# Optimization experiments

Measured on AMD Instinct MI355X. Metric: run time of the kernel, lower is better.

## Reference

```python
import jax, jax.numpy as jnp
import numpy as np
import math

B, T, N, E = 16, 12, 2000, 8000
D, GAT_HEADS, NHEAD, FF, L, HORIZON = 64, 4, 4, 128, 2, 3
M = B * N  # batched node count


def setup_inputs() -> dict:
    key = jax.random.key(0)
    ks = jax.random.split(key, 16)

    def nrm(k, shape, s=0.1):
        return jax.random.normal(k, shape, jnp.float32) * s

    return dict(
        x_seq=jax.random.normal(ks[0], (B, T, N), jnp.float32),
        edge_index=jax.random.randint(ks[1], (2, E), 0, N),
        # GATConv 1: in_dim=1 -> 4 heads x 8 = 32
        W1=nrm(ks[2], (1, 32)),
        att_src1=nrm(ks[3], (GAT_HEADS, 8)),
        att_dst1=nrm(ks[4], (GAT_HEADS, 8)),
        b1=jnp.zeros((32,), jnp.float32),
        # GATConv 2: 32 -> 4 heads x 16 = 64
        W2=nrm(ks[5], (32, 64)),
        att_src2=nrm(ks[6], (GAT_HEADS, 16)),
        att_dst2=nrm(ks[7], (GAT_HEADS, 16)),
        b2=jnp.zeros((64,), jnp.float32),
        # TransformerEncoder (post-LN, relu), stacked over L layers
        Wqkv=nrm(ks[8], (L, 3 * D, D)), bqkv=jnp.zeros((L, 3 * D), jnp.float32),
        Wo=nrm(ks[9], (L, D, D)), bo=jnp.zeros((L, D), jnp.float32),
        Wf1=nrm(ks[10], (L, FF, D)), bf1=jnp.zeros((L, FF), jnp.float32),
        Wf2=nrm(ks[11], (L, D, FF)), bf2=jnp.zeros((L, D), jnp.float32),
        g1=jnp.ones((L, D), jnp.float32), be1=jnp.zeros((L, D), jnp.float32),
        g2=jnp.ones((L, D), jnp.float32), be2=jnp.zeros((L, D), jnp.float32),
        # prediction head
        Wh=nrm(ks[12], (HORIZON, D)), bh=jnp.zeros((HORIZON,), jnp.float32),
    )


def _layer_norm(x, g, b, eps=1e-5):
    mu = x.mean(-1, keepdims=True)
    var = ((x - mu) ** 2).mean(-1, keepdims=True)
    return (x - mu) * jax.lax.rsqrt(var + eps) * g + b


def _gat(x, src, dst, W, a_src, a_dst, bias, H, C, num_nodes):
    # PyG GATConv (concat=True, eval mode). x: [M, in] -> [M, H*C]
    h = (x @ W).reshape(-1, H, C)                                  # [M,H,C]
    e = jax.nn.leaky_relu((h * a_src).sum(-1)[src] + (h * a_dst).sum(-1)[dst], 0.2)  # [Etot,H]
    m = jax.ops.segment_max(e, dst, num_segments=num_nodes)
    w = jnp.exp(e - m[dst])
    s = jax.ops.segment_sum(w, dst, num_segments=num_nodes)
    alpha = w / (s[dst] + 1e-16)
    out = jax.ops.segment_sum(h[src] * alpha[:, :, None], dst, num_segments=num_nodes)
    return out.reshape(-1, H * C) + bias


def _forward(x_seq, edge_index, W1, att_src1, att_dst1, b1, W2, att_src2, att_dst2, b2,
             Wqkv, bqkv, Wo, bo, Wf1, bf1, Wf2, bf2, g1, be1, g2, be2, Wh, bh):
    # batch edge index with per-graph node offsets, then add self loops (PyG default)
    offs = (jnp.arange(B) * N)[:, None]
    loops = jnp.arange(M)
    src = jnp.concatenate([(edge_index[0][None] + offs).reshape(-1), loops])
    dst = jnp.concatenate([(edge_index[1][None] + offs).reshape(-1), loops])

    xt = x_seq.transpose(1, 0, 2).reshape(T, M, 1)  # per-timestep node features

    def gnn_step(x):
        h = jax.nn.relu(_gat(x, src, dst, W1, att_src1, att_dst1, b1, GAT_HEADS, 8, M))
        return jax.nn.relu(_gat(h, src, dst, W2, att_src2, att_dst2, b2, GAT_HEADS, 16, M))

    seq = jax.vmap(gnn_step)(xt)  # [T, M, D]

    # sinusoidal positional encoding over time axis
    pos = jnp.arange(T, dtype=jnp.float32)[:, None]
    div = jnp.exp(jnp.arange(0, D, 2, dtype=jnp.float32) * (-math.log(10000.0) / D))
    pe = jnp.zeros((T, D), jnp.float32)
    pe = pe.at[:, 0::2].set(jnp.sin(pos * div)).at[:, 1::2].set(jnp.cos(pos * div))
    seq = seq + pe[:, None, :]

    hd = D // NHEAD
    scale = 1.0 / math.sqrt(hd)
    for i in range(L):  # post-LN transformer encoder layers
        qkv = seq @ Wqkv[i].T + bqkv[i]
        q, k, v = jnp.split(qkv, 3, axis=-1)
        q = q.reshape(T, M, NHEAD, hd)
        k = k.reshape(T, M, NHEAD, hd)
        v = v.reshape(T, M, NHEAD, hd)
        sc = jnp.einsum('tmhd,smhd->mhts', q, k) * scale  # [M,H,T,T]
        attn = jax.nn.softmax(sc, axis=-1)
        o = jnp.einsum('mhts,smhd->tmhd', attn, v).reshape(T, M, D)
        seq = _layer_norm(seq + (o @ Wo[i].T + bo[i]), g1[i], be1[i])
        ff = jax.nn.relu(seq @ Wf1[i].T + bf1[i]) @ Wf2[i].T + bf2[i]
        seq = _layer_norm(seq + ff, g2[i], be2[i])

    final = seq[-1]  # [M, D]
    return (final @ Wh.T + bh).reshape(B, N, HORIZON).transpose(0, 2, 1)  # [B, horizon, N]


def reference(x_seq, edge_index, W1, att_src1, att_dst1, b1, W2, att_src2, att_dst2, b2,
              Wqkv, bqkv, Wo, bo, Wf1, bf1, Wf2, bf2, g1, be1, g2, be2, Wh, bh):
    return _forward(x_seq, edge_index, W1, att_src1, att_dst1, b1, W2, att_src2, att_dst2, b2,
                    Wqkv, bqkv, Wo, bo, Wf1, bf1, Wf2, bf2, g1, be1, g2, be2, Wh, bh)
```

## Files before the change

### kernel.cpp

```cpp
#include <hip/hip_runtime.h>
#include <hip/hip_bf16.h>

#define B_ 16
#define T_ 12
#define N_ 2000
#define E_ 8000
#define M_ 32000
#define ETOT (B_*E_ + M_)
#define D_ 64

typedef __hip_bfloat16 bf16;
typedef unsigned short u16;
typedef __attribute__((ext_vector_type(8))) _Float16 half8;
typedef __attribute__((ext_vector_type(2))) _Float16 h2v;
typedef __attribute__((ext_vector_type(4))) float f32x4;

__device__ __forceinline__ float bfu(u16 u){ return __uint_as_float(((unsigned int)u)<<16); }
__device__ __forceinline__ u16 f2bu(float f){
  unsigned int x = __float_as_uint(f);
  x += 0x7FFFu + ((x >> 16) & 1u);
  return (u16)(x >> 16);
}
__device__ __forceinline__ u16 f2h(float f){
  _Float16 h = (_Float16)f; u16 r; __builtin_memcpy(&r, &h, 2); return r;
}
__device__ __forceinline__ float h2f(u16 u){
  _Float16 h; __builtin_memcpy(&h, &u, 2); return (float)h;
}
__device__ __forceinline__ h2v u2h(unsigned u){ h2v r; __builtin_memcpy(&r,&u,4); return r; }

__global__ void k_prep(const float* __restrict__ Wqkv, const float* __restrict__ Wo,
                       const float* __restrict__ Wf1, const float* __restrict__ Wf2,
                       u16* __restrict__ wqB, u16* __restrict__ woB,
                       u16* __restrict__ w1B, u16* __restrict__ w2B,
                       float* __restrict__ peT){
  int i = blockIdx.x*256 + threadIdx.x;
  if(i < 24576){
    int l=i/12288, r=i-l*12288;
    int nt=r>>10, r2=r&1023, c=r2>>9, r3=r2&511, lane=r3>>3, jj=r3&7;
    int m=lane&15, q=lane>>4;
    wqB[i] = f2h(Wqkv[l*12288 + (nt*16+m)*64 + c*32 + q*8 + jj]);
  } else if(i < 32768){
    int k2=i-24576;
    int l=k2>>12, r=k2&4095;
    int nt=r>>10, r2=r&1023, c=r2>>9, r3=r2&511, lane=r3>>3, jj=r3&7;
    int m=lane&15, q=lane>>4;
    woB[k2] = f2h(Wo[l*4096 + (nt*16+m)*64 + c*32 + q*8 + jj]);
  } else if(i < 49152){
    int k2=i-32768;
    int l=k2>>13, r=k2&8191;
    int nt=r>>10, r2=r&1023, c=r2>>9, r3=r2&511, lane=r3>>3, jj=r3&7;
    int m=lane&15, q=lane>>4;
    w1B[k2] = f2h(Wf1[l*8192 + (nt*16+m)*64 + c*32 + q*8 + jj]);
  } else if(i < 65536){
    int k2=i-49152;
    int l=k2>>13, r=k2&8191;
    int nt=r>>11, r2=r&2047, c=r2>>9, r3=r2&511, lane=r3>>3, jj=r3&7;
    int m=lane&15, q=lane>>4;
    w2B[k2] = f2h(Wf2[l*8192 + (nt*16+m)*128 + c*32 + q*8 + jj]);
  } else {
    int i2 = i - 65536;
    if(i2 < 768){
      int t=i2>>6, ch=i2&63;
      float ang = (float)t * __expf(-0.14391156463f * (float)(ch & ~1));
      peT[i2] = (ch&1) ? __cosf(ang) : __sinf(ang);
    }
  }
}

__global__ void k_hist(const int* __restrict__ ei, int* __restrict__ deg){
  int e = blockIdx.x*256 + threadIdx.x; if(e>=ETOT) return;
  int dst;
  if (e < B_*E_){ int b = e / E_; int k = e - b*E_; dst = ei[E_ + k] + b*N_; }
  else dst = e - B_*E_;
  atomicAdd(&deg[dst], 1);
}

__global__ void k_scan1(const int* __restrict__ deg, int* __restrict__ offs, int* __restrict__ bsums){
  __shared__ int s[256];
  int tid = threadIdx.x; int g = blockIdx.x*256 + tid;
  s[tid] = deg[g]; __syncthreads();
  for(int off=1; off<256; off<<=1){
    int a = (tid>=off) ? s[tid-off] : 0; __syncthreads();
    s[tid] += a; __syncthreads();
  }
  offs[g+1] = s[tid];
  if(tid==255) bsums[blockIdx.x] = s[255];
}

__global__ void k_scan2(const int* __restrict__ bsums, int* __restrict__ boffs){
  __shared__ int s[128];
  int tid = threadIdx.x;
  int v = (tid<125) ? bsums[tid] : 0;
  s[tid] = v; __syncthreads();
  for(int off=1; off<128; off<<=1){
    int a = (tid>=off) ? s[tid-off] : 0; __syncthreads();
    s[tid] += a; __syncthreads();
  }
  if(tid<125) boffs[tid] = s[tid] - v;
}

__global__ void k_scan3(int* __restrict__ offs, const int* __restrict__ boffs){
  int tid = threadIdx.x; int g = blockIdx.x*256 + tid;
  offs[g+1] += boffs[blockIdx.x];
  if(g==0) offs[0]=0;
}

__global__ void k_scatter(const int* __restrict__ ei, const int* __restrict__ offs,
                          int* __restrict__ cursor, int* __restrict__ csr){
  int e = blockIdx.x*256 + threadIdx.x; if(e>=ETOT) return;
  int srcl, dst;
  if (e < B_*E_){ int b=e/E_; int k=e-b*E_; srcl=ei[k]; dst=ei[E_+k]+b*N_; }
  else { dst = e - B_*E_; int b=dst/N_; srcl = dst - b*N_; }
  int pos = atomicAdd(&cursor[dst], 1);
  csr[offs[dst]+pos] = srcl;
}

__global__ __launch_bounds__(256) void k_gat12(
  const float* __restrict__ x_seq, const float* __restrict__ W1,
  const float* __restrict__ as1, const float* __restrict__ ad1, const float* __restrict__ b1,
  const float* __restrict__ W2, const float* __restrict__ as2, const float* __restrict__ ad2,
  const int* __restrict__ offs, const int* __restrict__ csr,
  u16* __restrict__ h2u, float* __restrict__ asc, float* __restrict__ adc)
{
  __shared__ float W2s[2048];
  __shared__ float a2s[64], a2d[64];
  int tid = threadIdx.x;
  for(int i=tid;i<2048;i+=256) W2s[i]=W2[i];
  if(tid<64){ a2s[tid]=as2[tid]; a2d[tid]=ad2[tid]; }
  __syncthreads();

  int t = blockIdx.y;
  int id = blockIdx.x*256 + tid;
  int m = id>>2, l4 = id&3;

  float sS[4], sD[4];
  #pragma unroll
  for(int h=0;h<4;h++){
    float a=0.f, d=0.f;
    #pragma unroll
    for(int c=0;c<8;c++){ float w=W1[h*8+c]; a+=w*as1[h*8+c]; d+=w*ad1[h*8+c]; }
    sS[h]=a; sD[h]=d;
  }
  unsigned um=(unsigned)m, b=um/N_, n=um-b*N_;
  const float* xsl = x_seq + (size_t)(b*T_+t)*N_;
  float xm = xsl[n];
  int e0=offs[m], e1=offs[m+1];
  float sum[4]={0,0,0,0}, ax[4]={0,0,0,0};
  for(int e=e0+l4; e<e1; e+=4){
    float xv = xsl[csr[e]];
    #pragma unroll
    for(int h=0;h<4;h++){
      float ee = xv*sS[h] + xm*sD[h]; ee = ee>0.f ? ee : 0.2f*ee;
      float w = __expf(ee); sum[h]+=w; ax[h]+=w*xv;
    }
  }
  float A[4];
  #pragma unroll
  for(int h=0;h<4;h++){
    sum[h] += __shfl_xor(sum[h],1); sum[h] += __shfl_xor(sum[h],2);
    ax[h]  += __shfl_xor(ax[h],1);  ax[h]  += __shfl_xor(ax[h],2);
    A[h] = ax[h]/(sum[h]+1e-16f);
  }

  float acc[16];
  #pragma unroll
  for(int c=0;c<16;c++) acc[c]=0.f;
  #pragma unroll
  for(int k=0;k<32;k++){
    int hs = k>>3;
    float v = A[hs]*W1[k] + b1[k]; v = v>0.f ? v : 0.f;
    #pragma unroll
    for(int c=0;c<16;c++) acc[c] += v*W2s[k*64 + l4*16 + c];
  }
  uint2* hp = (uint2*)(h2u + ((size_t)t*M_ + m)*64 + l4*16);
  #pragma unroll
  for(int c2=0;c2<4;c2++){
    uint2 p;
    p.x = (unsigned)f2bu(acc[4*c2+0]) | ((unsigned)f2bu(acc[4*c2+1])<<16);
    p.y = (unsigned)f2bu(acc[4*c2+2]) | ((unsigned)f2bu(acc[4*c2+3])<<16);
    hp[c2] = p;
  }
  float ss=0.f, sd=0.f;
  #pragma unroll
  for(int c=0;c<16;c++){ ss += acc[c]*a2s[l4*16+c]; sd += acc[c]*a2d[l4*16+c]; }
  asc[((size_t)t*M_+m)*4+l4]=ss; adc[((size_t)t*M_+m)*4+l4]=sd;
}

__global__ __launch_bounds__(256) void k_gat2b(
  const u16* __restrict__ h2u, const float* __restrict__ asc, const float* __restrict__ adc,
  const float* __restrict__ b2, const int* __restrict__ offs, const int* __restrict__ csr,
  const float* __restrict__ peT, u16* __restrict__ seq)
{
  int t = blockIdx.y;
  int id = blockIdx.x*256 + threadIdx.x;
  int m = id>>2, h = id&3;
  unsigned um=(unsigned)m, b=um/N_;
  size_t base_s = (size_t)t*M_ + (size_t)b*N_;
  float am = adc[((size_t)t*M_+m)*4+h];
  int e0=offs[m], e1=offs[m+1];
  float sum=0.f;
  float A[16];
  #pragma unroll
  for(int c=0;c<16;c++) A[c]=0.f;
  for(int e=e0;e<e1;e++){
    size_t s = base_s + (unsigned)csr[e];
    float ee = asc[s*4+h] + am; ee = ee>0.f ? ee : 0.2f*ee;
    float w = __expf(ee); sum += w;
    const uint2* hp = (const uint2*)(h2u + s*64 + h*16);
    #pragma unroll
    for(int c2=0;c2<4;c2++){
      uint2 p = hp[c2];
      A[4*c2+0] += w*bfu((u16)(p.x));
      A[4*c2+1] += w*bfu((u16)(p.x>>16));
      A[4*c2+2] += w*bfu((u16)(p.y));
      A[4*c2+3] += w*bfu((u16)(p.y>>16));
    }
  }
  float inv = 1.f/(sum + 1e-16f);
  #pragma unroll
  for(int c=0;c<16;c++){
    int ch = h*16 + c;
    float v = A[c]*inv + b2[ch]; v = v>0.f ? v : 0.f;
    seq[((size_t)t*M_ + m)*64 + ch] = f2h(v + peT[t*64+ch]);
  }
}

__global__ __launch_bounds__(192) void k_layer2(
  u16* __restrict__ seq,
  const u16* __restrict__ wqB, const u16* __restrict__ woB,
  const u16* __restrict__ w1B, const u16* __restrict__ w2B,
  const float* __restrict__ bqkv, const float* __restrict__ bo,
  const float* __restrict__ bf1,  const float* __restrict__ bf2,
  const float* __restrict__ g1,   const float* __restrict__ be1,
  const float* __restrict__ g2,   const float* __restrict__ be2)
{
  __shared__ __align__(16) u16 X[3456];
  __shared__ __align__(16) u16 QKV[10368];
  u16* Hd = QKV + 3456;
  int tid=threadIdx.x, w=tid>>6, lane=tid&63;
  int m=lane&15, q=lane>>4;
  int r = w*16 + m;

  int trr[4]; size_t base_rr[4];
  #pragma unroll
  for(int rg=0;rg<4;rg++){
    int rc = w*16 + q*4 + rg;
    int nn = rc/12; trr[rg] = rc - nn*12;
    base_rr[rg] = ((size_t)trr[rg]*M_ + (size_t)blockIdx.x*4 + nn)*64;
  }

  #pragma unroll
  for(int rr=0; rr<16; rr++){
    int row = w*16+rr;
    int nn = row/12, tt = row-nn*12;
    X[row*72+lane] = seq[((size_t)tt*M_ + (size_t)blockIdx.x*4+nn)*64 + lane];
  }

  #pragma unroll 1
  for(int l=0; l<2; l++){
    const half8* wqv = (const half8*)(wqB + (size_t)l*12288);
    const half8* wov = (const half8*)(woB + (size_t)l*4096);
    const half8* w1v = (const half8*)(w1B + (size_t)l*8192);
    const half8* w2v = (const half8*)(w2B + (size_t)l*8192);
    const float* bq = bqkv + l*192;
    const float* boL = bo + l*64;
    const float* b1L = bf1 + l*128;
    const float* b2L = bf2 + l*64;
    const float* g1L = g1 + l*64, *be1L = be1 + l*64;
    const float* g2L = g2 + l*64, *be2L = be2 + l*64;

    half8 xa0 = *(const half8*)&X[r*72 + q*8];
    half8 xa1 = *(const half8*)&X[r*72 + 32 + q*8];
    #pragma unroll
    for(int nt=0; nt<12; nt++){
      f32x4 acc={0.f,0.f,0.f,0.f};
      acc = __builtin_amdgcn_mfma_f32_16x16x32_f16(xa0, wqv[(nt*2+0)*64+lane], acc,0,0,0);
      acc = __builtin_amdgcn_mfma_f32_16x16x32_f16(xa1, wqv[(nt*2+1)*64+lane], acc,0,0,0);
      int cg = nt*16+m; float bias = bq[cg];
      int s = nt>>2, lc = cg&63;
      #pragma unroll
      for(int rg=0;rg<4;rg++){
        int row = w*16 + q*4 + rg;
        QKV[s*3456 + row*72 + lc] = f2h(acc[rg]+bias);
      }
    }
    __syncthreads();

    {
      int an = tid/48, rem = tid - an*48;
      int ah = rem/12, at = rem - ah*12;
      u16* qrow = &QKV[(an*12+at)*72 + ah*16];
      uint4 qa = ((const uint4*)qrow)[0], qb = ((const uint4*)qrow)[1];
      float s[12];
      #pragma unroll
      for(int t2=0;t2<12;t2++){
        const uint4* kp = (const uint4*)&QKV[3456 + (an*12+t2)*72 + ah*16];
        uint4 ka=kp[0], kb=kp[1];
        float d=0.f;
        d=__builtin_amdgcn_fdot2(u2h(qa.x),u2h(ka.x),d,false);
        d=__builtin_amdgcn_fdot2(u2h(qa.y),u2h(ka.y),d,false);
        d=__builtin_amdgcn_fdot2(u2h(qa.z),u2h(ka.z),d,false);
        d=__builtin_amdgcn_fdot2(u2h(qa.w),u2h(ka.w),d,false);
        d=__builtin_amdgcn_fdot2(u2h(qb.x),u2h(kb.x),d,false);
        d=__builtin_amdgcn_fdot2(u2h(qb.y),u2h(kb.y),d,false);
        d=__builtin_amdgcn_fdot2(u2h(qb.z),u2h(kb.z),d,false);
        d=__builtin_amdgcn_fdot2(u2h(qb.w),u2h(kb.w),d,false);
        s[t2] = d*0.25f;
      }
      float mx=s[0];
      #pragma unroll
      for(int t2=1;t2<12;t2++) mx=fmaxf(mx,s[t2]);
      float sum=0.f;
      #pragma unroll
      for(int t2=0;t2<12;t2++){ s[t2]=__expf(s[t2]-mx); sum+=s[t2]; }
      float inv=1.f/sum;
      half8 o0, o1;
      #pragma unroll
      for(int i=0;i<8;i++){ o0[i]=(_Float16)0.f; o1[i]=(_Float16)0.f; }
      #pragma unroll
      for(int t2=0;t2<12;t2++){
        const half8* vr = (const half8*)&QKV[6912 + (an*12+t2)*72 + ah*16];
        _Float16 wh = (_Float16)s[t2];
        o0 += vr[0]*wh; o1 += vr[1]*wh;
      }
      _Float16 ih = (_Float16)inv;
      ((half8*)qrow)[0]=o0*ih; ((half8*)qrow)[1]=o1*ih;
    }
    __syncthreads();

    half8 oa0 = *(const half8*)&QKV[r*72 + q*8];
    half8 oa1 = *(const half8*)&QKV[r*72 + 32 + q*8];
    float y[4][4];
    #pragma unroll
    for(int nt=0;nt<4;nt++){
      f32x4 acc={0.f,0.f,0.f,0.f};
      acc = __builtin_amdgcn_mfma_f32_16x16x32_f16(oa0, wov[(nt*2+0)*64+lane], acc,0,0,0);
      acc = __builtin_amdgcn_mfma_f32_16x16x32_f16(oa1, wov[(nt*2+1)*64+lane], acc,0,0,0);
      int col=nt*16+m; float bias=boL[col];
      #pragma unroll
      for(int rg=0;rg<4;rg++)
        y[nt][rg] = acc[rg] + bias + h2f(X[(w*16+q*4+rg)*72 + col]);
    }
    float mu[4], rs[4];
    #pragma unroll
    for(int rg=0;rg<4;rg++){
      float sm=(y[0][rg]+y[1][rg])+(y[2][rg]+y[3][rg]);
      sm+=__shfl_xor(sm,1); sm+=__shfl_xor(sm,2); sm+=__shfl_xor(sm,4); sm+=__shfl_xor(sm,8);
      mu[rg]=sm*(1.f/64.f);
      float d0=y[0][rg]-mu[rg],d1=y[1][rg]-mu[rg],d2=y[2][rg]-mu[rg],d3=y[3][rg]-mu[rg];
      float vv=(d0*d0+d1*d1)+(d2*d2+d3*d3);
      vv+=__shfl_xor(vv,1); vv+=__shfl_xor(vv,2); vv+=__shfl_xor(vv,4); vv+=__shfl_xor(vv,8);
      rs[rg]=rsqrtf(vv*(1.f/64.f)+1e-5f);
    }
    #pragma unroll
    for(int nt=0;nt<4;nt++){
      int col=nt*16+m; float g=g1L[col], be=be1L[col];
      #pragma unroll
      for(int rg=0;rg<4;rg++){
        float v=(y[nt][rg]-mu[rg])*rs[rg]*g+be;
        y[nt][rg]=v;
        QKV[(w*16+q*4+rg)*72 + col]=f2h(v);
      }
    }

    half8 ya0 = *(const half8*)&QKV[r*72 + q*8];
    half8 ya1 = *(const half8*)&QKV[r*72 + 32 + q*8];
    #pragma unroll
    for(int nt=0;nt<8;nt++){
      f32x4 acc={0.f,0.f,0.f,0.f};
      acc = __builtin_amdgcn_mfma_f32_16x16x32_f16(ya0, w1v[(nt*2+0)*64+lane], acc,0,0,0);
      acc = __builtin_amdgcn_mfma_f32_16x16x32_f16(ya1, w1v[(nt*2+1)*64+lane], acc,0,0,0);
      float bias=b1L[nt*16+m];
      #pragma unroll
      for(int rg=0;rg<4;rg++)
        Hd[(w*16+q*4+rg)*136 + nt*16+m] = f2h(fmaxf(acc[rg]+bias, 0.f));
    }

    half8 ha[4];
    #pragma unroll
    for(int c=0;c<4;c++)
      ha[c] = *(const half8*)&Hd[r*136 + c*32 + q*8];
    #pragma unroll
    for(int nt=0;nt<4;nt++){
      f32x4 acc={0.f,0.f,0.f,0.f};
      #pragma unroll
      for(int c=0;c<4;c++)
        acc = __builtin_amdgcn_mfma_f32_16x16x32_f16(ha[c], w2v[(nt*4+c)*64+lane], acc,0,0,0);
      int col=nt*16+m; float bias=b2L[col];
      #pragma unroll
      for(int rg=0;rg<4;rg++)
        y[nt][rg] = acc[rg] + bias + y[nt][rg];
    }
    #pragma unroll
    for(int rg=0;rg<4;rg++){
      float sm=(y[0][rg]+y[1][rg])+(y[2][rg]+y[3][rg]);
      sm+=__shfl_xor(sm,1); sm+=__shfl_xor(sm,2); sm+=__shfl_xor(sm,4); sm+=__shfl_xor(sm,8);
      mu[rg]=sm*(1.f/64.f);
      float d0=y[0][rg]-mu[rg],d1=y[1][rg]-mu[rg],d2=y[2][rg]-mu[rg],d3=y[3][rg]-mu[rg];
      float vv=(d0*d0+d1*d1)+(d2*d2+d3*d3);
      vv+=__shfl_xor(vv,1); vv+=__shfl_xor(vv,2); vv+=__shfl_xor(vv,4); vv+=__shfl_xor(vv,8);
      rs[rg]=rsqrtf(vv*(1.f/64.f)+1e-5f);
    }
    if(l==0){
      #pragma unroll
      for(int nt=0;nt<4;nt++){
        int col=nt*16+m; float g=g2L[col], be=be2L[col];
        #pragma unroll
        for(int rg=0;rg<4;rg++)
          X[(w*16+q*4+rg)*72 + col] = f2h((y[nt][rg]-mu[rg])*rs[rg]*g + be);
      }
      __syncthreads();
    } else {
      #pragma unroll
      for(int nt=0;nt<4;nt++){
        int col=nt*16+m; float g=g2L[col], be=be2L[col];
        #pragma unroll
        for(int rg=0;rg<4;rg++){
          if(trr[rg]==11)
            seq[base_rr[rg] + col] = f2h((y[nt][rg]-mu[rg])*rs[rg]*g + be);
        }
      }
    }
  }
}

__global__ void k_head(const u16* __restrict__ seq, const float* __restrict__ Wh,
                       const float* __restrict__ bh, float* __restrict__ out){
  int m = blockIdx.x*256 + threadIdx.x; if(m>=M_) return;
  const u16* row = seq + ((size_t)11*M_ + m)*64;
  float a0=bh[0], a1=bh[1], a2=bh[2];
  #pragma unroll
  for(int d=0;d<64;d++){
    float x = h2f(row[d]);
    a0 += x*Wh[d]; a1 += x*Wh[64+d]; a2 += x*Wh[128+d];
  }
  unsigned b=(unsigned)m/N_, n=(unsigned)m-b*N_;
  out[(b*3+0)*N_+n] = a0;
  out[(b*3+1)*N_+n] = a1;
  out[(b*3+2)*N_+n] = a2;
}

extern "C" void kernel_launch(void* const* d_in, const int* in_sizes, int n_in,
                              void* d_out, int out_size, void* d_ws, size_t ws_size,
                              hipStream_t stream)
{
  const float* x_seq=(const float*)d_in[0];
  const int*   ei   =(const int*)d_in[1];
  const float* W1   =(const float*)d_in[2];
  const float* as1  =(const float*)d_in[3];
  const float* ad1  =(const float*)d_in[4];
  const float* b1   =(const float*)d_in[5];
  const float* W2   =(const float*)d_in[6];
  const float* as2  =(const float*)d_in[7];
  const float* ad2  =(const float*)d_in[8];
  const float* b2   =(const float*)d_in[9];
  const float* Wqkv =(const float*)d_in[10];
  const float* bqkv =(const float*)d_in[11];
  const float* Wo   =(const float*)d_in[12];
  const float* bo   =(const float*)d_in[13];
  const float* Wf1  =(const float*)d_in[14];
  const float* bf1p =(const float*)d_in[15];
  const float* Wf2  =(const float*)d_in[16];
  const float* bf2p =(const float*)d_in[17];
  const float* g1   =(const float*)d_in[18];
  const float* be1  =(const float*)d_in[19];
  const float* g2   =(const float*)d_in[20];
  const float* be2  =(const float*)d_in[21];
  const float* Wh   =(const float*)d_in[22];
  const float* bh   =(const float*)d_in[23];

  u16* seqh   = (u16*)d_ws;
  float* asc  = (float*)(seqh + 24576000);
  float* adc  = asc + 1536000;
  int* deg    = (int*)(adc + 1536000);
  int* cursor = deg + M_;
  int* offs   = cursor + M_;
  int* bsums  = offs + (M_ + 2);
  int* boffs  = bsums + 128;
  int* csr    = boffs + 128;
  u16* h2u    = (u16*)(csr + ETOT);
  u16* wqB    = h2u + (size_t)T_*M_*64;
  u16* woB    = wqB + 24576;
  u16* w1B    = woB + 8192;
  u16* w2B    = w1B + 16384;
  float* peT  = (float*)(w2B + 16384);

  k_prep   <<<dim3(260), dim3(256), 0, stream>>>(Wqkv, Wo, Wf1, Wf2, wqB, woB, w1B, w2B, peT);

  hipMemsetAsync(deg, 0, (size_t)2*M_*sizeof(int), stream);
  k_hist   <<<dim3((ETOT+255)/256), dim3(256), 0, stream>>>(ei, deg);
  k_scan1  <<<dim3(125), dim3(256), 0, stream>>>(deg, offs, bsums);
  k_scan2  <<<dim3(1),   dim3(128), 0, stream>>>(bsums, boffs);
  k_scan3  <<<dim3(125), dim3(256), 0, stream>>>(offs, boffs);
  k_scatter<<<dim3((ETOT+255)/256), dim3(256), 0, stream>>>(ei, offs, cursor, csr);

  k_gat12<<<dim3(500,T_), dim3(256), 0, stream>>>(x_seq, W1, as1, ad1, b1,
                                                  W2, as2, ad2, offs, csr, h2u, asc, adc);
  k_gat2b<<<dim3(500,T_), dim3(256), 0, stream>>>(h2u, asc, adc, b2, offs, csr, peT, seqh);

  k_layer2<<<dim3(8000), dim3(192), 0, stream>>>(seqh,
      wqB, woB, w1B, w2B,
      bqkv, bo, bf1p, bf2p,
      g1, be1, g2, be2);

  k_head<<<dim3(125), dim3(256), 0, stream>>>(seqh, Wh, bh, (float*)d_out);
}
```

Before: 402.7 us.

## Fuse prediction head into transformer layer kernel and vectorize sequence loads

The final-layer normalized output for the last timestep now goes straight into the 3-way prediction head inside k_layer2, using a cross-lane shuffle reduction. This removes the separate k_head launch and the write and re-read of the last-timestep sequence rows. The initial shared-memory fill also switches from per-element 16-bit loads to 16-byte uint4 loads. The fused head assumes the last timestep always lands at register-group index 3 of its row group, which holds only because 48 rows map evenly onto 12 timesteps.

```diff
diff --git a/kernel.cpp b/kernel.cpp
--- a/kernel.cpp
+++ b/kernel.cpp
@@ -227,13 +227,15 @@
 }
 
 __global__ __launch_bounds__(192) void k_layer2(
-  u16* __restrict__ seq,
+  const u16* __restrict__ seq,
   const u16* __restrict__ wqB, const u16* __restrict__ woB,
   const u16* __restrict__ w1B, const u16* __restrict__ w2B,
   const float* __restrict__ bqkv, const float* __restrict__ bo,
   const float* __restrict__ bf1,  const float* __restrict__ bf2,
   const float* __restrict__ g1,   const float* __restrict__ be1,
-  const float* __restrict__ g2,   const float* __restrict__ be2)
+  const float* __restrict__ g2,   const float* __restrict__ be2,
+  const float* __restrict__ Wh,   const float* __restrict__ bh,
+  float* __restrict__ out)
 {
   __shared__ __align__(16) u16 X[3456];
   __shared__ __align__(16) u16 QKV[10368];
@@ -242,19 +244,13 @@
   int m=lane&15, q=lane>>4;
   int r = w*16 + m;
 
-  int trr[4]; size_t base_rr[4];
-  #pragma unroll
-  for(int rg=0;rg<4;rg++){
-    int rc = w*16 + q*4 + rg;
-    int nn = rc/12; trr[rg] = rc - nn*12;
-    base_rr[rg] = ((size_t)trr[rg]*M_ + (size_t)blockIdx.x*4 + nn)*64;
-  }
-
-  #pragma unroll
-  for(int rr=0; rr<16; rr++){
-    int row = w*16+rr;
+  #pragma unroll
+  for(int half=0; half<2; half++){
+    int rr = half*8 + (lane>>3);
+    int row = w*16 + rr;
     int nn = row/12, tt = row-nn*12;
-    X[row*72+lane] = seq[((size_t)tt*M_ + (size_t)blockIdx.x*4+nn)*64 + lane];
+    const uint4* src = (const uint4*)(seq + ((size_t)tt*M_ + (size_t)blockIdx.x*4+nn)*64) + (lane&7);
+    *((uint4*)&X[row*72] + (lane&7)) = *src;
   }
 
   #pragma unroll 1
@@ -412,33 +408,28 @@
       }
       __syncthreads();
     } else {
-      #pragma unroll
-      for(int nt=0;nt<4;nt++){
-        int col=nt*16+m; float g=g2L[col], be=be2L[col];
+      int rc = w*16 + q*4 + 3;
+      int nn = rc/12;
+      if(rc - nn*12 == 11){
+        float vfin[4];
         #pragma unroll
-        for(int rg=0;rg<4;rg++){
-          if(trr[rg]==11)
-            seq[base_rr[rg] + col] = f2h((y[nt][rg]-mu[rg])*rs[rg]*g + be);
+        for(int nt=0;nt<4;nt++){
+          int col=nt*16+m;
+          vfin[nt] = (y[nt][3]-mu[3])*rs[3]*g2L[col] + be2L[col];
         }
-      }
-    }
-  }
-}
-
-__global__ void k_head(const u16* __restrict__ seq, const float* __restrict__ Wh,
-                       const float* __restrict__ bh, float* __restrict__ out){
-  int m = blockIdx.x*256 + threadIdx.x; if(m>=M_) return;
-  const u16* row = seq + ((size_t)11*M_ + m)*64;
-  float a0=bh[0], a1=bh[1], a2=bh[2];
-  #pragma unroll
-  for(int d=0;d<64;d++){
-    float x = h2f(row[d]);
-    a0 += x*Wh[d]; a1 += x*Wh[64+d]; a2 += x*Wh[128+d];
-  }
-  unsigned b=(unsigned)m/N_, n=(unsigned)m-b*N_;
-  out[(b*3+0)*N_+n] = a0;
-  out[(b*3+1)*N_+n] = a1;
-  out[(b*3+2)*N_+n] = a2;
+        int gm = blockIdx.x*4 + nn;
+        unsigned bb=(unsigned)gm/N_, n2=(unsigned)gm-bb*N_;
+        #pragma unroll
+        for(int h3=0;h3<3;h3++){
+          float p = vfin[0]*Wh[h3*64+m]    + vfin[1]*Wh[h3*64+16+m]
+                  + vfin[2]*Wh[h3*64+32+m] + vfin[3]*Wh[h3*64+48+m];
+          p += __shfl_xor(p,1); p += __shfl_xor(p,2);
+          p += __shfl_xor(p,4); p += __shfl_xor(p,8);
+          if(m==0) out[(bb*3+h3)*N_+n2] = p + bh[h3];
+        }
+      }
+    }
+  }
 }
 
 extern "C" void kernel_launch(void* const* d_in, const int* in_sizes, int n_in,
@@ -502,7 +493,6 @@
   k_layer2<<<dim3(8000), dim3(192), 0, stream>>>(seqh,
       wqB, woB, w1B, w2B,
       bqkv, bo, bf1p, bf2p,
-      g1, be1, g2, be2);
-
-  k_head<<<dim3(125), dim3(256), 0, stream>>>(seqh, Wh, bh, (float*)d_out);
-}
+      g1, be1, g2, be2,
+      Wh, bh, (float*)d_out);
+}
```

New measurement: 400.8 us. No clear change (-0.5%).
